# Kernel tuning notes

Hardware: AMD Instinct MI355X
Metric: run time of the kernel (lower is better)

The kernel has to match this reference:

```python
import jax, jax.numpy as jnp
import numpy as np

N, IN_CH, OUT_CH = 100000, 512, 512


def setup_inputs() -> dict:
    key = jax.random.key(0)
    k1, k2, k3, k4 = jax.random.split(key, 4)
    # Xavier-uniform bounds: sqrt(6/(fan_in+fan_out)); Im uses gain=0.1
    bound = float(np.sqrt(6.0 / (IN_CH + OUT_CH)))
    x_re = jax.random.normal(k1, (N, IN_CH), dtype=jnp.float32)
    x_im = jax.random.normal(k2, (N, IN_CH), dtype=jnp.float32)
    Re = jax.random.uniform(k3, (OUT_CH, IN_CH), dtype=jnp.float32, minval=-bound, maxval=bound)
    Im = jax.random.uniform(k4, (OUT_CH, IN_CH), dtype=jnp.float32, minval=-0.1 * bound, maxval=0.1 * bound)
    return {"x_re": x_re, "x_im": x_im, "Re": Re, "Im": Im}


def reference(x_re, x_im, Re, Im):
    # Complex linear: out = x @ (Re + i*Im)^T, summed over in_channels.
    # Equivalent to torch.sum(x[:,None,:] * W[None,:,:], dim=2) but as GEMMs.
    out_re = jnp.einsum('ni,oi->no', x_re, Re) - jnp.einsum('ni,oi->no', x_im, Im)
    out_im = jnp.einsum('ni,oi->no', x_re, Im) + jnp.einsum('ni,oi->no', x_im, Re)
    return jnp.stack([out_re, out_im])  # (2, N, out_channels): real, imag
```

## Files before the change

kernel.cpp:

```cpp
#include <hip/hip_runtime.h>
#include <hip/hip_bf16.h>
#include <cstdint>

#define NROWS 100000
#define MPAD  100096
#define KDIM  1024
#define MTILES 782

typedef __attribute__((ext_vector_type(8))) __bf16 bf16x8;
typedef __attribute__((ext_vector_type(4))) float  f32x4;

__device__ __forceinline__ uint16_t f2bf(float f) {
    union { float f; uint32_t u; } v; v.f = f;
    uint32_t u = v.u;
    u += 0x7FFFu + ((u >> 16) & 1u);
    return (uint16_t)(u >> 16);
}

__device__ __forceinline__ void async16(const uint16_t* g, uint16_t* l) {
    __builtin_amdgcn_global_load_lds(
        (const __attribute__((address_space(1))) uint32_t*)g,
        (__attribute__((address_space(3))) uint32_t*)l,
        16, 0, 0);
}

__global__ __launch_bounds__(256) void pack_a_kernel(
        const float* __restrict__ xre, const float* __restrict__ xim,
        uint16_t* __restrict__ A) {
    int c = blockIdx.x * 256 + threadIdx.x;
    int n = c >> 7;
    int j = c & 127;
    uint32_t p0 = 0, p1 = 0, p2 = 0, p3 = 0;
    if (n < NROWS) {
        const float* src = (j < 64) ? (xre + (size_t)n * 512 + (size_t)j * 8)
                                    : (xim + (size_t)n * 512 + (size_t)(j - 64) * 8);
        float4 a = ((const float4*)src)[0];
        float4 b = ((const float4*)src)[1];
        p0 = (uint32_t)f2bf(a.x) | ((uint32_t)f2bf(a.y) << 16);
        p1 = (uint32_t)f2bf(a.z) | ((uint32_t)f2bf(a.w) << 16);
        p2 = (uint32_t)f2bf(b.x) | ((uint32_t)f2bf(b.y) << 16);
        p3 = (uint32_t)f2bf(b.z) | ((uint32_t)f2bf(b.w) << 16);
    }
    uint4 v; v.x = p0; v.y = p1; v.z = p2; v.w = p3;
    *(uint4*)(A + (size_t)c * 8) = v;
}

__global__ __launch_bounds__(256) void pack_b_kernel(
        const float* __restrict__ Re, const float* __restrict__ Im,
        uint16_t* __restrict__ Bt) {
    int c  = blockIdx.x * 256 + threadIdx.x;
    int oc = c >> 7;
    int j  = c & 127;
    const float* src;
    float sgn = 1.0f;
    if (oc < 512) {
        if (j < 64) { src = Re + (size_t)oc * 512 + (size_t)j * 8; }
        else        { src = Im + (size_t)oc * 512 + (size_t)(j - 64) * 8; sgn = -1.0f; }
    } else {
        int o = oc - 512;
        if (j < 64) { src = Im + (size_t)o * 512 + (size_t)j * 8; }
        else        { src = Re + (size_t)o * 512 + (size_t)(j - 64) * 8; }
    }
    float4 a = ((const float4*)src)[0];
    float4 b = ((const float4*)src)[1];
    uint32_t p0 = (uint32_t)f2bf(sgn * a.x) | ((uint32_t)f2bf(sgn * a.y) << 16);
    uint32_t p1 = (uint32_t)f2bf(sgn * a.z) | ((uint32_t)f2bf(sgn * a.w) << 16);
    uint32_t p2 = (uint32_t)f2bf(sgn * b.x) | ((uint32_t)f2bf(sgn * b.y) << 16);
    uint32_t p3 = (uint32_t)f2bf(sgn * b.z) | ((uint32_t)f2bf(sgn * b.w) << 16);
    uint4 v; v.x = p0; v.y = p1; v.z = p2; v.w = p3;
    *(uint4*)(Bt + (size_t)c * 8) = v;
}

__global__ __launch_bounds__(256) void gemm_kernel(
        const uint16_t* __restrict__ A, const uint16_t* __restrict__ Bt,
        float* __restrict__ C) {
    __shared__ uint16_t As[128 * 32];
    __shared__ uint16_t Bs[128 * 32];

    const int t    = threadIdx.x;
    const int wave = t >> 6;
    const int lane = t & 63;
    const int q    = lane >> 4;
    const int r16  = lane & 15;
    const int wm   = wave >> 1;
    const int wn   = wave & 1;

    const int colTile = blockIdx.x;
    const int rowTile = blockIdx.y;

    const size_t aRow0 = (size_t)rowTile * 128;
    const size_t bRow0 = (size_t)colTile * 128;

    const int g0 = t, g1 = t + 256;
    const int row0 = g0 >> 2, kk0 = (g0 & 3) ^ (row0 & 3);
    const int row1 = g1 >> 2, kk1 = (g1 & 3) ^ (row1 & 3);

    const uint16_t* gA0 = A  + (aRow0 + row0) * KDIM + kk0 * 8;
    const uint16_t* gA1 = A  + (aRow0 + row1) * KDIM + kk1 * 8;
    const uint16_t* gB0 = Bt + (bRow0 + row0) * KDIM + kk0 * 8;
    const uint16_t* gB1 = Bt + (bRow0 + row1) * KDIM + kk1 * 8;
    uint16_t* lA0 = As + g0 * 8;
    uint16_t* lA1 = As + g1 * 8;
    uint16_t* lB0 = Bs + g0 * 8;
    uint16_t* lB1 = Bs + g1 * 8;

    int gra[4], grb[4];
#pragma unroll
    for (int mi = 0; mi < 4; ++mi) {
        int row = wm * 64 + mi * 16 + r16;
        gra[mi] = row * 4 + (q ^ (row & 3));
    }
#pragma unroll
    for (int ni = 0; ni < 4; ++ni) {
        int row = wn * 64 + ni * 16 + r16;
        grb[ni] = row * 4 + (q ^ (row & 3));
    }

    f32x4 acc[4][4] = {};

    for (int kt = 0; kt < 32; ++kt) {
        const size_t koff = (size_t)kt * 32;
        async16(gA0 + koff, lA0);
        async16(gA1 + koff, lA1);
        async16(gB0 + koff, lB0);
        async16(gB1 + koff, lB1);
        __syncthreads();

        bf16x8 af[4], bfr[4];
#pragma unroll
        for (int mi = 0; mi < 4; ++mi)
            af[mi] = *(const bf16x8*)(As + gra[mi] * 8);
#pragma unroll
        for (int ni = 0; ni < 4; ++ni)
            bfr[ni] = *(const bf16x8*)(Bs + grb[ni] * 8);

#pragma unroll
        for (int mi = 0; mi < 4; ++mi)
#pragma unroll
            for (int ni = 0; ni < 4; ++ni)
                acc[mi][ni] = __builtin_amdgcn_mfma_f32_16x16x32_bf16(
                    af[mi], bfr[ni], acc[mi][ni], 0, 0, 0);

        __syncthreads();
    }

    const size_t outHalf = (colTile < 4) ? 0 : (size_t)NROWS * 512;
    const int cbase = (colTile & 3) * 128 + wn * 64;
#pragma unroll
    for (int mi = 0; mi < 4; ++mi) {
        int rbase = rowTile * 128 + wm * 64 + mi * 16 + q * 4;
#pragma unroll
        for (int ni = 0; ni < 4; ++ni) {
            int col = cbase + ni * 16 + r16;
#pragma unroll
            for (int r = 0; r < 4; ++r) {
                int row = rbase + r;
                if (row < NROWS)
                    C[outHalf + (size_t)row * 512 + col] = acc[mi][ni][r];
            }
        }
    }
}

__global__ void fallback_kernel(const float* __restrict__ xre,
                                const float* __restrict__ xim,
                                const float* __restrict__ Re,
                                const float* __restrict__ Im,
                                float* __restrict__ out) {
    __shared__ float sre[512], sim[512];
    int n = blockIdx.x;
    for (int i = threadIdx.x; i < 512; i += 256) {
        sre[i] = xre[(size_t)n * 512 + i];
        sim[i] = xim[(size_t)n * 512 + i];
    }
    __syncthreads();
    for (int o = threadIdx.x; o < 512; o += 256) {
        float are = 0.f, aim = 0.f;
        for (int k = 0; k < 512; ++k) {
            float wr = Re[(size_t)o * 512 + k], wi = Im[(size_t)o * 512 + k];
            float xr = sre[k], xi = sim[k];
            are += xr * wr - xi * wi;
            aim += xr * wi + xi * wr;
        }
        out[(size_t)n * 512 + o] = are;
        out[(size_t)NROWS * 512 + (size_t)n * 512 + o] = aim;
    }
}

extern "C" void kernel_launch(void* const* d_in, const int* in_sizes, int n_in,
                              void* d_out, int out_size, void* d_ws, size_t ws_size,
                              hipStream_t stream) {
    const float* xre = (const float*)d_in[0];
    const float* xim = (const float*)d_in[1];
    const float* Re  = (const float*)d_in[2];
    const float* Im  = (const float*)d_in[3];
    float* out = (float*)d_out;

    const size_t aBytes = (size_t)MPAD * KDIM * 2;
    const size_t bBytes = (size_t)1024 * KDIM * 2;
    if (ws_size >= aBytes + bBytes) {
        uint16_t* A  = (uint16_t*)d_ws;
        uint16_t* Bt = (uint16_t*)((char*)d_ws + aBytes);
        pack_a_kernel<<<(MPAD * 128) / 256, 256, 0, stream>>>(xre, xim, A);
        pack_b_kernel<<<(1024 * 128) / 256, 256, 0, stream>>>(Re, Im, Bt);
        dim3 grid(8, MTILES);
        gemm_kernel<<<grid, 256, 0, stream>>>(A, Bt, out);
    } else {
        fallback_kernel<<<NROWS, 256, 0, stream>>>(xre, xim, Re, Im, out);
    }
}
```

Measured before the change: 1.019 ms.

## Fuse fp32-to-bf16 A conversion into GEMM with double-buffered BK=64 pipeline

After: 919.7 us. -9.8%, faster.

```diff
diff --git a/kernel.cpp b/kernel.cpp
--- a/kernel.cpp
+++ b/kernel.cpp
@@ -2,10 +2,14 @@
 #include <hip/hip_bf16.h>
 #include <cstdint>
 
-#define NROWS 100000
-#define MPAD  100096
-#define KDIM  1024
+#define NROWS  100000
+#define KDIM   1024
+#define BM     128
+#define BN     128
+#define BK     64
 #define MTILES 782
+#define NTILES 8
+#define NBLK   (MTILES * NTILES)
 
 typedef __attribute__((ext_vector_type(8))) __bf16 bf16x8;
 typedef __attribute__((ext_vector_type(4))) float  f32x4;
@@ -17,32 +21,17 @@
     return (uint16_t)(u >> 16);
 }
 
+__device__ __forceinline__ uint32_t pkbf(float lo, float hi) {
+    uint32_t r;
+    asm("v_cvt_pk_bf16_f32 %0, %1, %2" : "=v"(r) : "v"(lo), "v"(hi));
+    return r;
+}
+
 __device__ __forceinline__ void async16(const uint16_t* g, uint16_t* l) {
     __builtin_amdgcn_global_load_lds(
         (const __attribute__((address_space(1))) uint32_t*)g,
         (__attribute__((address_space(3))) uint32_t*)l,
         16, 0, 0);
-}
-
-__global__ __launch_bounds__(256) void pack_a_kernel(
-        const float* __restrict__ xre, const float* __restrict__ xim,
-        uint16_t* __restrict__ A) {
-    int c = blockIdx.x * 256 + threadIdx.x;
-    int n = c >> 7;
-    int j = c & 127;
-    uint32_t p0 = 0, p1 = 0, p2 = 0, p3 = 0;
-    if (n < NROWS) {
-        const float* src = (j < 64) ? (xre + (size_t)n * 512 + (size_t)j * 8)
-                                    : (xim + (size_t)n * 512 + (size_t)(j - 64) * 8);
-        float4 a = ((const float4*)src)[0];
-        float4 b = ((const float4*)src)[1];
-        p0 = (uint32_t)f2bf(a.x) | ((uint32_t)f2bf(a.y) << 16);
-        p1 = (uint32_t)f2bf(a.z) | ((uint32_t)f2bf(a.w) << 16);
-        p2 = (uint32_t)f2bf(b.x) | ((uint32_t)f2bf(b.y) << 16);
-        p3 = (uint32_t)f2bf(b.z) | ((uint32_t)f2bf(b.w) << 16);
-    }
-    uint4 v; v.x = p0; v.y = p1; v.z = p2; v.w = p3;
-    *(uint4*)(A + (size_t)c * 8) = v;
 }
 
 __global__ __launch_bounds__(256) void pack_b_kernel(
@@ -71,11 +60,11 @@
     *(uint4*)(Bt + (size_t)c * 8) = v;
 }
 
-__global__ __launch_bounds__(256) void gemm_kernel(
-        const uint16_t* __restrict__ A, const uint16_t* __restrict__ Bt,
-        float* __restrict__ C) {
-    __shared__ uint16_t As[128 * 32];
-    __shared__ uint16_t Bs[128 * 32];
+__global__ __launch_bounds__(256) void gemm_fused(
+        const float* __restrict__ xre, const float* __restrict__ xim,
+        const uint16_t* __restrict__ Bt, float* __restrict__ C) {
+    __shared__ uint16_t As[2 * BM * BK];
+    __shared__ uint16_t Bs[2 * BN * BK];
 
     const int t    = threadIdx.x;
     const int wave = t >> 6;
@@ -85,70 +74,140 @@
     const int wm   = wave >> 1;
     const int wn   = wave & 1;
 
-    const int colTile = blockIdx.x;
-    const int rowTile = blockIdx.y;
-
-    const size_t aRow0 = (size_t)rowTile * 128;
-    const size_t bRow0 = (size_t)colTile * 128;
-
-    const int g0 = t, g1 = t + 256;
-    const int row0 = g0 >> 2, kk0 = (g0 & 3) ^ (row0 & 3);
-    const int row1 = g1 >> 2, kk1 = (g1 & 3) ^ (row1 & 3);
-
-    const uint16_t* gA0 = A  + (aRow0 + row0) * KDIM + kk0 * 8;
-    const uint16_t* gA1 = A  + (aRow0 + row1) * KDIM + kk1 * 8;
-    const uint16_t* gB0 = Bt + (bRow0 + row0) * KDIM + kk0 * 8;
-    const uint16_t* gB1 = Bt + (bRow0 + row1) * KDIM + kk1 * 8;
-    uint16_t* lA0 = As + g0 * 8;
-    uint16_t* lA1 = As + g1 * 8;
-    uint16_t* lB0 = Bs + g0 * 8;
-    uint16_t* lB1 = Bs + g1 * 8;
-
-    int gra[4], grb[4];
-#pragma unroll
-    for (int mi = 0; mi < 4; ++mi) {
-        int row = wm * 64 + mi * 16 + r16;
-        gra[mi] = row * 4 + (q ^ (row & 3));
-    }
-#pragma unroll
-    for (int ni = 0; ni < 4; ++ni) {
-        int row = wn * 64 + ni * 16 + r16;
-        grb[ni] = row * 4 + (q ^ (row & 3));
+    const int bid     = blockIdx.x;
+    const int newid   = (bid & 7) * (NBLK / 8) + (bid >> 3);
+    const int colTile = newid & 7;
+    const int rowTile = newid >> 3;
+
+    const int aRow0 = rowTile * BM;
+    const int bRow0 = colTile * BN;
+
+    int  aLds[4];
+    int  aOff[4];
+    bool aOk[4];
+    const uint16_t* bPtr[4];
+    int  bLds[4];
+#pragma unroll
+    for (int i = 0; i < 4; ++i) {
+        int g   = i * 256 + t;
+        int row = g >> 3;
+        int kk  = g & 7;
+        int swz = kk ^ (row & 7);
+        aLds[i] = (row * 8 + swz) * 8;
+        int grow = aRow0 + row;
+        aOk[i]  = grow < NROWS;
+        aOff[i] = grow * 512 + kk * 8;
+        bPtr[i] = Bt + (size_t)(bRow0 + row) * KDIM + swz * 8;
+        bLds[i] = g * 8;
+    }
+
+    int gra[4][2], grb[4][2];
+#pragma unroll
+    for (int x = 0; x < 4; ++x) {
+#pragma unroll
+        for (int ks = 0; ks < 2; ++ks) {
+            int rowA = wm * 64 + x * 16 + r16;
+            gra[x][ks] = (rowA * 8 + ((ks * 4 + q) ^ (rowA & 7))) * 8;
+            int rowB = wn * 64 + x * 16 + r16;
+            grb[x][ks] = (rowB * 8 + ((ks * 4 + q) ^ (rowB & 7))) * 8;
+        }
     }
 
     f32x4 acc[4][4] = {};
 
-    for (int kt = 0; kt < 32; ++kt) {
-        const size_t koff = (size_t)kt * 32;
-        async16(gA0 + koff, lA0);
-        async16(gA1 + koff, lA1);
-        async16(gB0 + koff, lB0);
-        async16(gB1 + koff, lB1);
+    {
+        float4 va[4], vb[4];
+#pragma unroll
+        for (int i = 0; i < 4; ++i) {
+            if (aOk[i]) {
+                const float4* p = (const float4*)(xre + aOff[i]);
+                va[i] = p[0]; vb[i] = p[1];
+            } else {
+                va[i] = make_float4(0.f, 0.f, 0.f, 0.f);
+                vb[i] = make_float4(0.f, 0.f, 0.f, 0.f);
+            }
+        }
+#pragma unroll
+        for (int i = 0; i < 4; ++i)
+            async16(bPtr[i], Bs + bLds[i]);
+#pragma unroll
+        for (int i = 0; i < 4; ++i) {
+            uint4 u;
+            u.x = pkbf(va[i].x, va[i].y);
+            u.y = pkbf(va[i].z, va[i].w);
+            u.z = pkbf(vb[i].x, vb[i].y);
+            u.w = pkbf(vb[i].z, vb[i].w);
+            *(uint4*)(As + aLds[i]) = u;
+        }
         __syncthreads();
-
-        bf16x8 af[4], bfr[4];
+    }
+
+    int cur = 0;
+    for (int kt = 0; kt < 16; ++kt) {
+        const int nxt = cur ^ 1;
+
+        float4 va[4], vb[4];
+        if (kt < 15) {
+            const float* src = (kt + 1 < 8) ? xre : xim;
+            const int kb = ((kt + 1) & 7) * 64;
+#pragma unroll
+            for (int i = 0; i < 4; ++i) {
+                if (aOk[i]) {
+                    const float4* p = (const float4*)(src + aOff[i] + kb);
+                    va[i] = p[0]; vb[i] = p[1];
+                } else {
+                    va[i] = make_float4(0.f, 0.f, 0.f, 0.f);
+                    vb[i] = make_float4(0.f, 0.f, 0.f, 0.f);
+                }
+            }
+            const size_t gk = (size_t)(kt + 1) * 64;
+#pragma unroll
+            for (int i = 0; i < 4; ++i)
+                async16(bPtr[i] + gk, Bs + nxt * (BN * BK) + bLds[i]);
+        }
+
+        const uint16_t* Ab = As + cur * (BM * BK);
+        const uint16_t* Bb = Bs + cur * (BN * BK);
+        bf16x8 af[4][2], bfr[4][2];
+#pragma unroll
+        for (int x = 0; x < 4; ++x) {
+#pragma unroll
+            for (int ks = 0; ks < 2; ++ks) {
+                af[x][ks]  = *(const bf16x8*)(Ab + gra[x][ks]);
+                bfr[x][ks] = *(const bf16x8*)(Bb + grb[x][ks]);
+            }
+        }
 #pragma unroll
         for (int mi = 0; mi < 4; ++mi)
-            af[mi] = *(const bf16x8*)(As + gra[mi] * 8);
-#pragma unroll
-        for (int ni = 0; ni < 4; ++ni)
-            bfr[ni] = *(const bf16x8*)(Bs + grb[ni] * 8);
-
-#pragma unroll
-        for (int mi = 0; mi < 4; ++mi)
-#pragma unroll
-            for (int ni = 0; ni < 4; ++ni)
+#pragma unroll
+            for (int ni = 0; ni < 4; ++ni) {
                 acc[mi][ni] = __builtin_amdgcn_mfma_f32_16x16x32_bf16(
-                    af[mi], bfr[ni], acc[mi][ni], 0, 0, 0);
-
+                    af[mi][0], bfr[ni][0], acc[mi][ni], 0, 0, 0);
+                acc[mi][ni] = __builtin_amdgcn_mfma_f32_16x16x32_bf16(
+                    af[mi][1], bfr[ni][1], acc[mi][ni], 0, 0, 0);
+            }
+
+        if (kt < 15) {
+            uint16_t* Ad = As + nxt * (BM * BK);
+#pragma unroll
+            for (int i = 0; i < 4; ++i) {
+                uint4 u;
+                u.x = pkbf(va[i].x, va[i].y);
+                u.y = pkbf(va[i].z, va[i].w);
+                u.z = pkbf(vb[i].x, vb[i].y);
+                u.w = pkbf(vb[i].z, vb[i].w);
+                *(uint4*)(Ad + aLds[i]) = u;
+            }
+        }
         __syncthreads();
+        cur = nxt;
     }
 
     const size_t outHalf = (colTile < 4) ? 0 : (size_t)NROWS * 512;
     const int cbase = (colTile & 3) * 128 + wn * 64;
 #pragma unroll
     for (int mi = 0; mi < 4; ++mi) {
-        int rbase = rowTile * 128 + wm * 64 + mi * 16 + q * 4;
+        int rbase = aRow0 + wm * 64 + mi * 16 + q * 4;
 #pragma unroll
         for (int ni = 0; ni < 4; ++ni) {
             int col = cbase + ni * 16 + r16;
@@ -196,15 +255,11 @@
     const float* Im  = (const float*)d_in[3];
     float* out = (float*)d_out;
 
-    const size_t aBytes = (size_t)MPAD * KDIM * 2;
     const size_t bBytes = (size_t)1024 * KDIM * 2;
-    if (ws_size >= aBytes + bBytes) {
-        uint16_t* A  = (uint16_t*)d_ws;
-        uint16_t* Bt = (uint16_t*)((char*)d_ws + aBytes);
-        pack_a_kernel<<<(MPAD * 128) / 256, 256, 0, stream>>>(xre, xim, A);
+    if (ws_size >= bBytes) {
+        uint16_t* Bt = (uint16_t*)d_ws;
         pack_b_kernel<<<(1024 * 128) / 256, 256, 0, stream>>>(Re, Im, Bt);
-        dim3 grid(8, MTILES);
-        gemm_kernel<<<grid, 256, 0, stream>>>(A, Bt, out);
+        gemm_fused<<<NBLK, 256, 0, stream>>>(xre, xim, Bt, out);
     } else {
         fallback_kernel<<<NROWS, 256, 0, stream>>>(xre, xim, Re, Im, out);
     }
```

## Rewrite GEMM as 256x256 tile, 8-wave double-buffered pipeline with XCD-aware block mapping

Applied to the files above, without the earlier changes.

New measurement: 867.3 us. 1.18x faster.

```diff
diff --git a/kernel.cpp b/kernel.cpp
--- a/kernel.cpp
+++ b/kernel.cpp
@@ -2,10 +2,12 @@
 #include <hip/hip_bf16.h>
 #include <cstdint>
 
-#define NROWS 100000
-#define MPAD  100096
-#define KDIM  1024
-#define MTILES 782
+#define NROWS  100000
+#define KDIM   1024
+#define MPAD   100096
+#define MTILES 391
+#define NTILES 4
+#define NBLK   (MTILES * NTILES)
 
 typedef __attribute__((ext_vector_type(8))) __bf16 bf16x8;
 typedef __attribute__((ext_vector_type(4))) float  f32x4;
@@ -71,92 +73,162 @@
     *(uint4*)(Bt + (size_t)c * 8) = v;
 }
 
-__global__ __launch_bounds__(256) void gemm_kernel(
+__global__ __launch_bounds__(512, 2) void gemm8(
         const uint16_t* __restrict__ A, const uint16_t* __restrict__ Bt,
         float* __restrict__ C) {
-    __shared__ uint16_t As[128 * 32];
-    __shared__ uint16_t Bs[128 * 32];
+    __shared__ uint16_t lds[65536];
 
     const int t    = threadIdx.x;
     const int wave = t >> 6;
     const int lane = t & 63;
     const int q    = lane >> 4;
     const int r16  = lane & 15;
-    const int wm   = wave >> 1;
-    const int wn   = wave & 1;
-
-    const int colTile = blockIdx.x;
-    const int rowTile = blockIdx.y;
-
-    const size_t aRow0 = (size_t)rowTile * 128;
-    const size_t bRow0 = (size_t)colTile * 128;
-
-    const int g0 = t, g1 = t + 256;
-    const int row0 = g0 >> 2, kk0 = (g0 & 3) ^ (row0 & 3);
-    const int row1 = g1 >> 2, kk1 = (g1 & 3) ^ (row1 & 3);
-
-    const uint16_t* gA0 = A  + (aRow0 + row0) * KDIM + kk0 * 8;
-    const uint16_t* gA1 = A  + (aRow0 + row1) * KDIM + kk1 * 8;
-    const uint16_t* gB0 = Bt + (bRow0 + row0) * KDIM + kk0 * 8;
-    const uint16_t* gB1 = Bt + (bRow0 + row1) * KDIM + kk1 * 8;
-    uint16_t* lA0 = As + g0 * 8;
-    uint16_t* lA1 = As + g1 * 8;
-    uint16_t* lB0 = Bs + g0 * 8;
-    uint16_t* lB1 = Bs + g1 * 8;
-
-    int gra[4], grb[4];
-#pragma unroll
-    for (int mi = 0; mi < 4; ++mi) {
-        int row = wm * 64 + mi * 16 + r16;
-        gra[mi] = row * 4 + (q ^ (row & 3));
-    }
-#pragma unroll
-    for (int ni = 0; ni < 4; ++ni) {
-        int row = wn * 64 + ni * 16 + r16;
-        grb[ni] = row * 4 + (q ^ (row & 3));
-    }
-
-    f32x4 acc[4][4] = {};
-
-    for (int kt = 0; kt < 32; ++kt) {
-        const size_t koff = (size_t)kt * 32;
-        async16(gA0 + koff, lA0);
-        async16(gA1 + koff, lA1);
-        async16(gB0 + koff, lB0);
-        async16(gB1 + koff, lB1);
-        __syncthreads();
-
-        bf16x8 af[4], bfr[4];
-#pragma unroll
-        for (int mi = 0; mi < 4; ++mi)
-            af[mi] = *(const bf16x8*)(As + gra[mi] * 8);
-#pragma unroll
-        for (int ni = 0; ni < 4; ++ni)
-            bfr[ni] = *(const bf16x8*)(Bs + grb[ni] * 8);
-
-#pragma unroll
-        for (int mi = 0; mi < 4; ++mi)
-#pragma unroll
-            for (int ni = 0; ni < 4; ++ni)
-                acc[mi][ni] = __builtin_amdgcn_mfma_f32_16x16x32_bf16(
-                    af[mi], bfr[ni], acc[mi][ni], 0, 0, 0);
-
-        __syncthreads();
-    }
-
-    const size_t outHalf = (colTile < 4) ? 0 : (size_t)NROWS * 512;
-    const int cbase = (colTile & 3) * 128 + wn * 64;
-#pragma unroll
-    for (int mi = 0; mi < 4; ++mi) {
-        int rbase = rowTile * 128 + wm * 64 + mi * 16 + q * 4;
-#pragma unroll
-        for (int ni = 0; ni < 4; ++ni) {
-            int col = cbase + ni * 16 + r16;
+    const int wm   = wave >> 2;
+    const int wn   = wave & 3;
+
+    const int bid  = blockIdx.x;
+    const int xcd  = bid & 7, lid = bid >> 3;
+    const int wgid = (xcd < 4 ? xcd * 196 : 784 + (xcd - 4) * 195) + lid;
+    const int colTile = wgid & 3;
+    const int rowTile = wgid >> 2;
+    const int aRow0   = rowTile * 256;
+
+    const int s7  = r16 & 7;
+    const int sA0 = r16 * 64 + ((q ^ s7) << 3);
+    const int sA1 = r16 * 64 + (((q + 4) ^ s7) << 3);
+
+    const int g0 = t, g1 = t + 512;
+    const int r0 = g0 >> 3, k0 = ((g0 & 7) ^ (r0 & 7)) << 3;
+    const int r1 = g1 >> 3, k1 = ((g1 & 7) ^ (r1 & 7)) << 3;
+    const int lA00 = g0 * 8,          lA01 = g1 * 8;
+    const int lA10 = 8192 + g0 * 8,   lA11 = 8192 + g1 * 8;
+    const int lB00 = 16384 + g0 * 8,  lB01 = 16384 + g1 * 8;
+    const int lB10 = 24576 + g0 * 8,  lB11 = 24576 + g1 * 8;
+    const uint16_t* pA00 = A  + (size_t)(aRow0 + r0) * KDIM + k0;
+    const uint16_t* pA01 = A  + (size_t)(aRow0 + r1) * KDIM + k1;
+    const uint16_t* pA10 = A  + (size_t)(aRow0 + 128 + r0) * KDIM + k0;
+    const uint16_t* pA11 = A  + (size_t)(aRow0 + 128 + r1) * KDIM + k1;
+    const uint16_t* pB00 = Bt + (size_t)(colTile * 256 + r0) * KDIM + k0;
+    const uint16_t* pB01 = Bt + (size_t)(colTile * 256 + r1) * KDIM + k1;
+    const uint16_t* pB10 = Bt + (size_t)(colTile * 256 + 128 + r0) * KDIM + k0;
+    const uint16_t* pB11 = Bt + (size_t)(colTile * 256 + 128 + r1) * KDIM + k1;
+
+    async16(pA00, lds + lA00); async16(pA01, lds + lA01);
+    async16(pA10, lds + lA10); async16(pA11, lds + lA11);
+    async16(pB00, lds + lB00); async16(pB01, lds + lB01);
+    async16(pB10, lds + lB10); async16(pB11, lds + lB11);
+    async16(pA00 + 64, lds + 32768 + lA00); async16(pA01 + 64, lds + 32768 + lA01);
+    async16(pA10 + 64, lds + 32768 + lA10); async16(pA11 + 64, lds + 32768 + lA11);
+    async16(pB00 + 64, lds + 32768 + lB00); async16(pB01 + 64, lds + 32768 + lB01);
+    async16(pB10 + 64, lds + 32768 + lB10); async16(pB11 + 64, lds + 32768 + lB11);
+    pA00 += 128; pA01 += 128; pA10 += 128; pA11 += 128;
+    pB00 += 128; pB01 += 128; pB10 += 128; pB11 += 128;
+    asm volatile("s_waitcnt vmcnt(8)" ::: "memory");
+    __builtin_amdgcn_s_barrier();
+
+    f32x4 acc[8][4] = {};
+
+#pragma unroll 2
+    for (int kt = 0; kt < 16; ++kt) {
+        const int bufO = (kt & 1) << 15;
+        const uint16_t* bA = lds + bufO + wm * 8192;
+        const uint16_t* bB = lds + bufO + 16384 + (wn >> 1) * 8192 + (wn & 1) * 4096;
+        uint16_t* ldsd = lds + bufO;
+
+        bf16x8 af[4][2], b0[2][2], b1[2][2];
+#pragma unroll
+        for (int mi = 0; mi < 4; ++mi) {
+            af[mi][0] = *(const bf16x8*)(bA + mi * 1024 + sA0);
+            af[mi][1] = *(const bf16x8*)(bA + mi * 1024 + sA1);
+        }
+#pragma unroll
+        for (int ni = 0; ni < 2; ++ni) {
+            b0[ni][0] = *(const bf16x8*)(bB + ni * 1024 + sA0);
+            b0[ni][1] = *(const bf16x8*)(bB + ni * 1024 + sA1);
+        }
+        __builtin_amdgcn_s_barrier();
+        __builtin_amdgcn_s_setprio(1);
+#pragma unroll
+        for (int mi = 0; mi < 4; ++mi)
+#pragma unroll
+            for (int nj = 0; nj < 2; ++nj) {
+                acc[mi][nj] = __builtin_amdgcn_mfma_f32_16x16x32_bf16(af[mi][0], b0[nj][0], acc[mi][nj], 0, 0, 0);
+                acc[mi][nj] = __builtin_amdgcn_mfma_f32_16x16x32_bf16(af[mi][1], b0[nj][1], acc[mi][nj], 0, 0, 0);
+            }
+        __builtin_amdgcn_s_setprio(0);
+        __builtin_amdgcn_s_barrier();
+#pragma unroll
+        for (int ni = 0; ni < 2; ++ni) {
+            b1[ni][0] = *(const bf16x8*)(bB + 2048 + ni * 1024 + sA0);
+            b1[ni][1] = *(const bf16x8*)(bB + 2048 + ni * 1024 + sA1);
+        }
+        __builtin_amdgcn_s_barrier();
+        __builtin_amdgcn_s_setprio(1);
+#pragma unroll
+        for (int mi = 0; mi < 4; ++mi)
+#pragma unroll
+            for (int nj = 0; nj < 2; ++nj) {
+                acc[mi][2 + nj] = __builtin_amdgcn_mfma_f32_16x16x32_bf16(af[mi][0], b1[nj][0], acc[mi][2 + nj], 0, 0, 0);
+                acc[mi][2 + nj] = __builtin_amdgcn_mfma_f32_16x16x32_bf16(af[mi][1], b1[nj][1], acc[mi][2 + nj], 0, 0, 0);
+            }
+        __builtin_amdgcn_s_setprio(0);
+        __builtin_amdgcn_s_barrier();
+#pragma unroll
+        for (int mi = 0; mi < 4; ++mi) {
+            af[mi][0] = *(const bf16x8*)(bA + 4096 + mi * 1024 + sA0);
+            af[mi][1] = *(const bf16x8*)(bA + 4096 + mi * 1024 + sA1);
+        }
+        if (kt < 14) {
+            __builtin_amdgcn_sched_barrier(0);
+            async16(pB00, ldsd + lB00); async16(pB01, ldsd + lB01);
+            async16(pB10, ldsd + lB10); async16(pB11, ldsd + lB11);
+        }
+        __builtin_amdgcn_s_barrier();
+        __builtin_amdgcn_s_setprio(1);
+#pragma unroll
+        for (int mi = 0; mi < 4; ++mi)
+#pragma unroll
+            for (int nj = 0; nj < 2; ++nj) {
+                acc[4 + mi][2 + nj] = __builtin_amdgcn_mfma_f32_16x16x32_bf16(af[mi][0], b1[nj][0], acc[4 + mi][2 + nj], 0, 0, 0);
+                acc[4 + mi][2 + nj] = __builtin_amdgcn_mfma_f32_16x16x32_bf16(af[mi][1], b1[nj][1], acc[4 + mi][2 + nj], 0, 0, 0);
+            }
+        __builtin_amdgcn_s_setprio(0);
+        __builtin_amdgcn_s_barrier();
+        if (kt < 14) {
+            __builtin_amdgcn_sched_barrier(0);
+            async16(pA00, ldsd + lA00); async16(pA01, ldsd + lA01);
+            async16(pA10, ldsd + lA10); async16(pA11, ldsd + lA11);
+            pA00 += 64; pA01 += 64; pA10 += 64; pA11 += 64;
+            pB00 += 64; pB01 += 64; pB10 += 64; pB11 += 64;
+        }
+        __builtin_amdgcn_s_barrier();
+        __builtin_amdgcn_s_setprio(1);
+#pragma unroll
+        for (int mi = 0; mi < 4; ++mi)
+#pragma unroll
+            for (int nj = 0; nj < 2; ++nj) {
+                acc[4 + mi][nj] = __builtin_amdgcn_mfma_f32_16x16x32_bf16(af[mi][0], b0[nj][0], acc[4 + mi][nj], 0, 0, 0);
+                acc[4 + mi][nj] = __builtin_amdgcn_mfma_f32_16x16x32_bf16(af[mi][1], b0[nj][1], acc[4 + mi][nj], 0, 0, 0);
+            }
+        __builtin_amdgcn_s_setprio(0);
+        if (kt < 14)       asm volatile("s_waitcnt vmcnt(8)" ::: "memory");
+        else if (kt == 14) asm volatile("s_waitcnt vmcnt(0)" ::: "memory");
+        __builtin_amdgcn_s_barrier();
+    }
+
+    const size_t outHalf = (colTile >= 2) ? (size_t)NROWS * 512 : 0;
+    const int cb = (colTile & 1) * 256 + wn * 64;
+#pragma unroll
+    for (int mi8 = 0; mi8 < 8; ++mi8) {
+        int rbase = aRow0 + wm * 128 + mi8 * 16 + q * 4;
+#pragma unroll
+        for (int nj = 0; nj < 4; ++nj) {
+            int col = cb + nj * 16 + r16;
 #pragma unroll
             for (int r = 0; r < 4; ++r) {
                 int row = rbase + r;
                 if (row < NROWS)
-                    C[outHalf + (size_t)row * 512 + col] = acc[mi][ni][r];
+                    C[outHalf + (size_t)row * 512 + col] = acc[mi8][nj][r];
             }
         }
     }
@@ -203,8 +275,7 @@
         uint16_t* Bt = (uint16_t*)((char*)d_ws + aBytes);
         pack_a_kernel<<<(MPAD * 128) / 256, 256, 0, stream>>>(xre, xim, A);
         pack_b_kernel<<<(1024 * 128) / 256, 256, 0, stream>>>(Re, Im, Bt);
-        dim3 grid(8, MTILES);
-        gemm_kernel<<<grid, 256, 0, stream>>>(A, Bt, out);
+        gemm8<<<NBLK, 512, 0, stream>>>(A, Bt, out);
     } else {
         fallback_kernel<<<NROWS, 256, 0, stream>>>(xre, xim, Re, Im, out);
     }
```
